# Optimization experiments

Hardware: AMD Instinct MI355X
Metric: run time of the kernel (lower is better)

The kernel has to match this reference:

```python
import jax, jax.numpy as jnp
import numpy as np

N_NODES = 100000   # number of graph nodes
N_EDGES = 1600000  # adjacency nnz (avg degree 16)
FEAT_NNZ = 1600000 # sparse feature nnz (~16 per node)
F_IN = 512
F_OUT = 128


def setup_inputs() -> dict:
    key = jax.random.key(0)
    k1, k2, k3, k4, k5, k6 = jax.random.split(key, 6)
    adj_indices = jax.random.randint(k1, (2, N_EDGES), 0, N_NODES, dtype=jnp.int64 if jax.config.jax_enable_x64 else jnp.int32)
    adj_values = jax.random.uniform(k2, (N_EDGES,), dtype=jnp.float32)
    feat_rows = jax.random.randint(k3, (FEAT_NNZ,), 0, N_NODES)
    feat_cols = jax.random.randint(k4, (FEAT_NNZ,), 0, F_IN)
    feat_values = jax.random.uniform(k5, (FEAT_NNZ,), dtype=jnp.float32)
    # xavier_uniform init of the dense weight, as in the torch module
    bound = float(np.sqrt(6.0 / (F_IN + F_OUT)))
    weight = jax.random.uniform(k6, (F_IN, F_OUT), dtype=jnp.float32, minval=-bound, maxval=bound)
    return {
        "adj_indices": adj_indices,
        "adj_values": adj_values,
        "feat_rows": feat_rows,
        "feat_cols": feat_cols,
        "feat_values": feat_values,
        "weight": weight,
        "num_nodes": N_NODES,
    }


def _spmm(rows, cols, vals, num_rows, dense):
    """COO sparse [num_rows, ?] @ dense [?, K] -> [num_rows, K]."""
    msgs = vals[:, None] * dense[cols]          # [nnz, K] gather + scale
    return jax.ops.segment_sum(msgs, rows, num_segments=num_rows)


def reference(adj_indices, adj_values, feat_rows, feat_cols, feat_values, weight, num_nodes):
    # spmm(features, W): sparse [N, F_in] @ [F_in, F_out]
    base_features = _spmm(feat_rows, feat_cols, feat_values, num_nodes, weight)
    # spmm(A_hat, base): sparse [N, N] @ [N, F_out]  -- neighbor aggregation
    out = _spmm(adj_indices[0], adj_indices[1], adj_values, num_nodes, base_features)
    return out
```

## Files before the change

kernel.cpp:

```cpp
#include <hip/hip_runtime.h>
#include <stdint.h>

#define N_NODES 100000
#define F_IN    512
#define F_OUT   128
#define BROWS   128
#define NBKT    ((N_NODES + BROWS - 1) / BROWS)
#define CAP     2560
#define EPB     4096
#define BR2     64
#define SCAP    1536

typedef unsigned short     u16;
typedef unsigned int       u32;
typedef unsigned long long u64;
typedef long long          i64;

__device__ __forceinline__ float b2f(u16 u) {
    union { u32 i; float f; } x; x.i = ((u32)u) << 16; return x.f;
}
__device__ __forceinline__ u16 f2b(float f) {
    u32 i = __float_as_uint(f);
    return (u16)((i + 0x7fffu + ((i >> 16) & 1u)) >> 16);
}
__device__ __forceinline__ float blo(u32 u) { return __uint_as_float(u << 16); }
__device__ __forceinline__ float bhi(u32 u) { return __uint_as_float(u & 0xFFFF0000u); }
__device__ __forceinline__ int ld_idx(const void* p, int i, int w64) {
    return w64 ? (int)((const i64*)p)[i] : ((const int*)p)[i];
}
__device__ __forceinline__ u16 ld_val_bf(const void* p, int i, int f32) {
    return f32 ? f2b(((const float*)p)[i]) : ((const u16*)p)[i];
}

__global__ void sniff_k(const u16* __restrict__ w, const u32* __restrict__ adj,
                        const u32* __restrict__ frows, int* __restrict__ flags,
                        int* __restrict__ gcurF, int* __restrict__ gcurA) {
    int t = threadIdx.x;
    if (t < 64) {
        int lane = t;
        u32 e0 = (w[lane]      >> 7) & 0xFF;
        u32 e1 = (w[64 + lane] >> 7) & 0xFF;
        u64 bad = __ballot((e0 > 0x7B) || (e1 > 0x7B));
        u64 za = __ballot(adj[2 * lane + 1] == 0u);
        u64 zf = __ballot(frows[2 * lane + 1] == 0u);
        if (lane == 0) {
            flags[0] = (bad != 0);
            flags[1] = (__popcll(za) >= 32);
            flags[2] = (__popcll(zf) >= 32);
        }
    }
    for (int i = t; i < NBKT; i += 256) { gcurF[i] = 0; gcurA[i] = 0; }
}

__global__ __launch_bounds__(256) void binFA_k(
        const void* __restrict__ frows, const void* __restrict__ fcols,
        const void* __restrict__ fvals, int M, int nFb,
        const void* __restrict__ adjbase, const void* __restrict__ avals, int E,
        const int* __restrict__ flags,
        int* __restrict__ gcurF, int* __restrict__ gcurA,
        u32* __restrict__ fbkt, u64* __restrict__ abkt) {
    __shared__ int hist[NBKT];
    __shared__ int hbase[NBKT];
    int t = threadIdx.x;
    for (int i = t; i < NBKT; i += 256) hist[i] = 0;
    __syncthreads();
    int f32 = flags[0];
    if ((int)blockIdx.x < nFb) {
        int f64 = flags[2];
        int start = blockIdx.x * EPB;
        int end = min(start + EPB, M);
        for (int i = start + t; i < end; i += 256)
            atomicAdd(&hist[ld_idx(frows, i, f64) >> 7], 1);
        __syncthreads();
        for (int i = t; i < NBKT; i += 256) {
            int h = hist[i];
            hbase[i] = h ? atomicAdd(&gcurF[i], h) : 0;
            hist[i] = 0;
        }
        __syncthreads();
        for (int i = start + t; i < end; i += 256) {
            int r = ld_idx(frows, i, f64);
            int c = ld_idx(fcols, i, f64);
            u32 v = ld_val_bf(fvals, i, f32);
            int b = r >> 7;
            int pos = hbase[b] + atomicAdd(&hist[b], 1);
            if (pos < CAP)
                fbkt[(size_t)b * CAP + pos] = (v << 16) | ((u32)(r & 127) << 9) | (u32)c;
        }
    } else {
        int a64 = flags[1];
        const void* acols = a64 ? (const void*)((const i64*)adjbase + E)
                                : (const void*)((const int*)adjbase + E);
        int start = ((int)blockIdx.x - nFb) * EPB;
        int end = min(start + EPB, E);
        for (int i = start + t; i < end; i += 256)
            atomicAdd(&hist[ld_idx(adjbase, i, a64) >> 7], 1);
        __syncthreads();
        for (int i = t; i < NBKT; i += 256) {
            int h = hist[i];
            hbase[i] = h ? atomicAdd(&gcurA[i], h) : 0;
            hist[i] = 0;
        }
        __syncthreads();
        for (int i = start + t; i < end; i += 256) {
            int r = ld_idx(adjbase, i, a64);
            int c = ld_idx(acols, i, a64);
            u64 v = ld_val_bf(avals, i, f32);
            int b = r >> 7;
            int pos = hbase[b] + atomicAdd(&hist[b], 1);
            if (pos < CAP)
                abkt[(size_t)b * CAP + pos] = (v << 24) | ((u64)(r & 127) << 17) | (u64)(u32)c;
        }
    }
}

__global__ __launch_bounds__(256, 8) void stage1_k(const int* __restrict__ cnt,
        const u32* __restrict__ bkts, const void* __restrict__ W,
        const int* __restrict__ flags, u16* __restrict__ base) {
    __shared__ u32 csr[SCAP];
    __shared__ int hcnt[BR2];
    __shared__ int roff[BR2 + 1];
    __shared__ int cur[BR2];
    int t = threadIdx.x;
    int b = blockIdx.x >> 1;
    int half = blockIdx.x & 1;
    int n = cnt[b]; if (n > CAP) n = CAP;
    const u32* ed = bkts + (size_t)b * CAP;
    if (t < BR2) hcnt[t] = 0;
    __syncthreads();
    for (int i = t; i < n; i += 256) {
        int rl = (ed[i] >> 9) & 0x7F;
        if ((rl >> 6) == half) atomicAdd(&hcnt[rl & 63], 1);
    }
    __syncthreads();
    if (t < 64) {
        int h = hcnt[t];
        int v = h;
        #pragma unroll
        for (int off = 1; off < 64; off <<= 1) {
            int u = __shfl_up(v, off);
            if (t >= off) v += u;
        }
        roff[t + 1] = v;
        cur[t] = v - h;
        if (t == 0) roff[0] = 0;
    }
    __syncthreads();
    for (int i = t; i < n; i += 256) {
        u32 p = ed[i];
        int rl = (p >> 9) & 0x7F;
        if ((rl >> 6) == half) {
            int pos = atomicAdd(&cur[rl & 63], 1);
            if (pos < SCAP) csr[pos] = p;
        }
    }
    __syncthreads();
    int wave = t >> 6, lane = t & 63, g = lane >> 4, l16 = lane & 15;
    int f32 = flags[0];
    #pragma unroll
    for (int set = 0; set < 4; ++set) {
        int row = set * 16 + wave * 4 + g;
        int s = roff[row], e = roff[row + 1];
        if (s > SCAP) s = SCAP;
        if (e > SCAP) e = SCAP;
        float a[8] = {0.f, 0.f, 0.f, 0.f, 0.f, 0.f, 0.f, 0.f};
        if (f32) {
            const float* Wf = (const float*)W;
            for (int j0 = s; j0 < e; j0 += 4) {
                u32 p[4]; float4 qa[4], qb[4];
                #pragma unroll
                for (int k = 0; k < 4; ++k) { int jk = j0 + k; p[k] = csr[jk < e ? jk : e - 1]; }
                #pragma unroll
                for (int k = 0; k < 4; ++k) {
                    const float* wp = Wf + (size_t)(p[k] & 0x1FF) * F_OUT + l16 * 8;
                    qa[k] = *(const float4*)wp;
                    qb[k] = *(const float4*)(wp + 4);
                }
                #pragma unroll
                for (int k = 0; k < 4; ++k) {
                    float v = (j0 + k < e) ? b2f((u16)(p[k] >> 16)) : 0.f;
                    a[0] += v * qa[k].x; a[1] += v * qa[k].y;
                    a[2] += v * qa[k].z; a[3] += v * qa[k].w;
                    a[4] += v * qb[k].x; a[5] += v * qb[k].y;
                    a[6] += v * qb[k].z; a[7] += v * qb[k].w;
                }
            }
        } else {
            const u16* Wb = (const u16*)W;
            for (int j0 = s; j0 < e; j0 += 4) {
                u32 p[4]; uint4 q[4];
                #pragma unroll
                for (int k = 0; k < 4; ++k) { int jk = j0 + k; p[k] = csr[jk < e ? jk : e - 1]; }
                #pragma unroll
                for (int k = 0; k < 4; ++k)
                    q[k] = *(const uint4*)(Wb + (size_t)(p[k] & 0x1FF) * F_OUT + l16 * 8);
                #pragma unroll
                for (int k = 0; k < 4; ++k) {
                    float v = (j0 + k < e) ? b2f((u16)(p[k] >> 16)) : 0.f;
                    a[0] += v * blo(q[k].x); a[1] += v * bhi(q[k].x);
                    a[2] += v * blo(q[k].y); a[3] += v * bhi(q[k].y);
                    a[4] += v * blo(q[k].z); a[5] += v * bhi(q[k].z);
                    a[6] += v * blo(q[k].w); a[7] += v * bhi(q[k].w);
                }
            }
        }
        int gr = b * BROWS + half * BR2 + row;
        if (gr < N_NODES) {
            uint4 o;
            o.x = (u32)f2b(a[0]) | ((u32)f2b(a[1]) << 16);
            o.y = (u32)f2b(a[2]) | ((u32)f2b(a[3]) << 16);
            o.z = (u32)f2b(a[4]) | ((u32)f2b(a[5]) << 16);
            o.w = (u32)f2b(a[6]) | ((u32)f2b(a[7]) << 16);
            *(uint4*)(base + (size_t)gr * F_OUT + l16 * 8) = o;
        }
    }
}

__global__ __launch_bounds__(256, 8) void stage2_k(const int* __restrict__ cnt,
        const u64* __restrict__ bkts, const u16* __restrict__ base,
        const int* __restrict__ flags, void* __restrict__ out) {
    __shared__ u64 csr[SCAP];
    __shared__ int hcnt[BR2];
    __shared__ int roff[BR2 + 1];
    __shared__ int cur[BR2];
    int t = threadIdx.x;
    int b = blockIdx.x >> 1;
    int half = blockIdx.x & 1;
    int n = cnt[b]; if (n > CAP) n = CAP;
    const u64* ed = bkts + (size_t)b * CAP;
    if (t < BR2) hcnt[t] = 0;
    __syncthreads();
    for (int i = t; i < n; i += 256) {
        int rl = (int)((ed[i] >> 17) & 0x7F);
        if ((rl >> 6) == half) atomicAdd(&hcnt[rl & 63], 1);
    }
    __syncthreads();
    if (t < 64) {
        int h = hcnt[t];
        int v = h;
        #pragma unroll
        for (int off = 1; off < 64; off <<= 1) {
            int u = __shfl_up(v, off);
            if (t >= off) v += u;
        }
        roff[t + 1] = v;
        cur[t] = v - h;
        if (t == 0) roff[0] = 0;
    }
    __syncthreads();
    for (int i = t; i < n; i += 256) {
        u64 p = ed[i];
        int rl = (int)((p >> 17) & 0x7F);
        if ((rl >> 6) == half) {
            int pos = atomicAdd(&cur[rl & 63], 1);
            if (pos < SCAP) csr[pos] = p;
        }
    }
    __syncthreads();
    int wave = t >> 6, lane = t & 63, g = lane >> 4, l16 = lane & 15;
    int f32o = flags[0];
    #pragma unroll
    for (int set = 0; set < 4; ++set) {
        int row = set * 16 + wave * 4 + g;
        int s = roff[row], e = roff[row + 1];
        if (s > SCAP) s = SCAP;
        if (e > SCAP) e = SCAP;
        float a[8] = {0.f, 0.f, 0.f, 0.f, 0.f, 0.f, 0.f, 0.f};
        for (int j0 = s; j0 < e; j0 += 4) {
            u64 p[4]; uint4 q[4];
            #pragma unroll
            for (int k = 0; k < 4; ++k) { int jk = j0 + k; p[k] = csr[jk < e ? jk : e - 1]; }
            #pragma unroll
            for (int k = 0; k < 4; ++k)
                q[k] = *(const uint4*)(base + (size_t)(u32)(p[k] & 0x1FFFF) * F_OUT + l16 * 8);
            #pragma unroll
            for (int k = 0; k < 4; ++k) {
                float v = (j0 + k < e) ? b2f((u16)(p[k] >> 24)) : 0.f;
                a[0] += v * blo(q[k].x); a[1] += v * bhi(q[k].x);
                a[2] += v * blo(q[k].y); a[3] += v * bhi(q[k].y);
                a[4] += v * blo(q[k].z); a[5] += v * bhi(q[k].z);
                a[6] += v * blo(q[k].w); a[7] += v * bhi(q[k].w);
            }
        }
        int gr = b * BROWS + half * BR2 + row;
        if (gr < N_NODES) {
            if (f32o) {
                float* op = (float*)out + (size_t)gr * F_OUT + l16 * 8;
                float4 o0, o1;
                o0.x = a[0]; o0.y = a[1]; o0.z = a[2]; o0.w = a[3];
                o1.x = a[4]; o1.y = a[5]; o1.z = a[6]; o1.w = a[7];
                *(float4*)op = o0;
                *(float4*)(op + 4) = o1;
            } else {
                uint4 o;
                o.x = (u32)f2b(a[0]) | ((u32)f2b(a[1]) << 16);
                o.y = (u32)f2b(a[2]) | ((u32)f2b(a[3]) << 16);
                o.z = (u32)f2b(a[4]) | ((u32)f2b(a[5]) << 16);
                o.w = (u32)f2b(a[6]) | ((u32)f2b(a[7]) << 16);
                *(uint4*)((u16*)out + (size_t)gr * F_OUT + l16 * 8) = o;
            }
        }
    }
}

extern "C" void kernel_launch(void* const* d_in, const int* in_sizes, int n_in,
                              void* d_out, int out_size, void* d_ws, size_t ws_size,
                              hipStream_t stream) {
    const void* adj_idx   = d_in[0];
    const void* adj_vals  = d_in[1];
    const void* feat_rows = d_in[2];
    const void* feat_cols = d_in[3];
    const void* feat_vals = d_in[4];
    const void* weight    = d_in[5];

    const int E = in_sizes[0] / 2;
    const int M = in_sizes[2];

    char* ws = (char*)d_ws;
    size_t o = 0;
    auto alloc = [&](size_t b) { size_t r = o; o += (b + 255) & ~(size_t)255; return r; };
    int* gcurF = (int*)(ws + alloc((size_t)NBKT * 4));
    int* gcurA = (int*)(ws + alloc((size_t)NBKT * 4));
    int* flags = (int*)(ws + alloc(4 * 4));
    u32* fbkt  = (u32*)(ws + alloc((size_t)NBKT * CAP * 4));
    u64* abkt  = (u64*)(ws + alloc((size_t)NBKT * CAP * 8));
    u16* base  = (u16*)(ws + alloc((size_t)N_NODES * F_OUT * 2));
    (void)ws_size;

    const int nFb = (M + EPB - 1) / EPB;
    const int nAb = (E + EPB - 1) / EPB;

    sniff_k<<<1, 256, 0, stream>>>((const u16*)weight, (const u32*)adj_idx,
                                   (const u32*)feat_rows, flags, gcurF, gcurA);
    binFA_k<<<nFb + nAb, 256, 0, stream>>>(feat_rows, feat_cols, feat_vals, M, nFb,
                                           adj_idx, adj_vals, E,
                                           flags, gcurF, gcurA, fbkt, abkt);
    stage1_k<<<2 * NBKT, 256, 0, stream>>>(gcurF, fbkt, weight, flags, base);
    stage2_k<<<2 * NBKT, 256, 0, stream>>>(gcurA, abkt, base, flags, d_out);
}
```

Measured before the change: 280.2 us.

## Stage binned entries in shared memory sorted by bucket before global scatter

The binning kernel now computes a block-local exclusive scan of the bucket histogram. It scatters each packed entry into a shared-memory buffer sorted by bucket, then writes to the global bucket arrays in sorted order, so consecutive threads mostly hit consecutive addresses. This replaces fully random global scatter writes with mostly coalesced ones. In exchange it uses about 40KB of extra LDS per block (u64 sort buffer plus u16 bucket tags), which lowers occupancy, and adds a scan plus another barrier pass.

```diff
diff --git a/kernel.cpp b/kernel.cpp
--- a/kernel.cpp
+++ b/kernel.cpp
@@ -59,12 +59,18 @@
         const int* __restrict__ flags,
         int* __restrict__ gcurF, int* __restrict__ gcurA,
         u32* __restrict__ fbkt, u64* __restrict__ abkt) {
+    __shared__ u64 sortA[EPB];
+    __shared__ u16 sbkt[EPB];
     __shared__ int hist[NBKT];
+    __shared__ int lbase[NBKT];
     __shared__ int hbase[NBKT];
+    __shared__ int wtot[4];
     int t = threadIdx.x;
+    int lane = t & 63, wv = t >> 6;
     for (int i = t; i < NBKT; i += 256) hist[i] = 0;
     __syncthreads();
     int f32 = flags[0];
+
     if ((int)blockIdx.x < nFb) {
         int f64 = flags[2];
         int start = blockIdx.x * EPB;
@@ -72,20 +78,55 @@
         for (int i = start + t; i < end; i += 256)
             atomicAdd(&hist[ld_idx(frows, i, f64) >> 7], 1);
         __syncthreads();
-        for (int i = t; i < NBKT; i += 256) {
-            int h = hist[i];
-            hbase[i] = h ? atomicAdd(&gcurF[i], h) : 0;
-            hist[i] = 0;
-        }
-        __syncthreads();
+        {
+            int b0 = t * 4;
+            int c0 = (b0 + 0 < NBKT) ? hist[b0 + 0] : 0;
+            int c1 = (b0 + 1 < NBKT) ? hist[b0 + 1] : 0;
+            int c2 = (b0 + 2 < NBKT) ? hist[b0 + 2] : 0;
+            int c3 = (b0 + 3 < NBKT) ? hist[b0 + 3] : 0;
+            int s = c0 + c1 + c2 + c3;
+            int v = s;
+            #pragma unroll
+            for (int off = 1; off < 64; off <<= 1) {
+                int u = __shfl_up(v, off);
+                if (lane >= off) v += u;
+            }
+            if (lane == 63) wtot[wv] = v;
+            __syncthreads();
+            int woff = 0;
+            #pragma unroll
+            for (int w = 0; w < 4; ++w) if (w < wv) woff += wtot[w];
+            int run = woff + v - s;
+            int cc[4] = {c0, c1, c2, c3};
+            #pragma unroll
+            for (int k = 0; k < 4; ++k) {
+                int bb = b0 + k;
+                if (bb < NBKT) {
+                    lbase[bb] = run;
+                    hist[bb] = run;
+                    hbase[bb] = cc[k] ? atomicAdd(&gcurF[bb], cc[k]) : 0;
+                    run += cc[k];
+                }
+            }
+        }
+        __syncthreads();
+        u32* sortF = (u32*)sortA;
         for (int i = start + t; i < end; i += 256) {
             int r = ld_idx(frows, i, f64);
             int c = ld_idx(fcols, i, f64);
             u32 v = ld_val_bf(fvals, i, f32);
             int b = r >> 7;
-            int pos = hbase[b] + atomicAdd(&hist[b], 1);
+            int pos = atomicAdd(&hist[b], 1);
+            sortF[pos] = (v << 16) | ((u32)(r & 127) << 9) | (u32)c;
+            sbkt[pos] = (u16)b;
+        }
+        __syncthreads();
+        int n = end - start;
+        for (int i = t; i < n; i += 256) {
+            int b = sbkt[i];
+            int pos = hbase[b] + (i - lbase[b]);
             if (pos < CAP)
-                fbkt[(size_t)b * CAP + pos] = (v << 16) | ((u32)(r & 127) << 9) | (u32)c;
+                fbkt[(size_t)b * CAP + pos] = sortF[i];
         }
     } else {
         int a64 = flags[1];
@@ -96,10 +137,36 @@
         for (int i = start + t; i < end; i += 256)
             atomicAdd(&hist[ld_idx(adjbase, i, a64) >> 7], 1);
         __syncthreads();
-        for (int i = t; i < NBKT; i += 256) {
-            int h = hist[i];
-            hbase[i] = h ? atomicAdd(&gcurA[i], h) : 0;
-            hist[i] = 0;
+        {
+            int b0 = t * 4;
+            int c0 = (b0 + 0 < NBKT) ? hist[b0 + 0] : 0;
+            int c1 = (b0 + 1 < NBKT) ? hist[b0 + 1] : 0;
+            int c2 = (b0 + 2 < NBKT) ? hist[b0 + 2] : 0;
+            int c3 = (b0 + 3 < NBKT) ? hist[b0 + 3] : 0;
+            int s = c0 + c1 + c2 + c3;
+            int v = s;
+            #pragma unroll
+            for (int off = 1; off < 64; off <<= 1) {
+                int u = __shfl_up(v, off);
+                if (lane >= off) v += u;
+            }
+            if (lane == 63) wtot[wv] = v;
+            __syncthreads();
+            int woff = 0;
+            #pragma unroll
+            for (int w = 0; w < 4; ++w) if (w < wv) woff += wtot[w];
+            int run = woff + v - s;
+            int cc[4] = {c0, c1, c2, c3};
+            #pragma unroll
+            for (int k = 0; k < 4; ++k) {
+                int bb = b0 + k;
+                if (bb < NBKT) {
+                    lbase[bb] = run;
+                    hist[bb] = run;
+                    hbase[bb] = cc[k] ? atomicAdd(&gcurA[bb], cc[k]) : 0;
+                    run += cc[k];
+                }
+            }
         }
         __syncthreads();
         for (int i = start + t; i < end; i += 256) {
@@ -107,9 +174,17 @@
             int c = ld_idx(acols, i, a64);
             u64 v = ld_val_bf(avals, i, f32);
             int b = r >> 7;
-            int pos = hbase[b] + atomicAdd(&hist[b], 1);
+            int pos = atomicAdd(&hist[b], 1);
+            sortA[pos] = (v << 24) | ((u64)(r & 127) << 17) | (u64)(u32)c;
+            sbkt[pos] = (u16)b;
+        }
+        __syncthreads();
+        int n = end - start;
+        for (int i = t; i < n; i += 256) {
+            int b = sbkt[i];
+            int pos = hbase[b] + (i - lbase[b]);
             if (pos < CAP)
-                abkt[(size_t)b * CAP + pos] = (v << 24) | ((u64)(r & 127) << 17) | (u64)(u32)c;
+                abkt[(size_t)b * CAP + pos] = sortA[i];
         }
     }
 }
```

Measured after the change: 280.7 us. No clear change (+0.2%).

## Split feature binning, fuse adjacency binning with stage1, use full-bucket 512-thread blocks

Applied to the files above, without the earlier changes.

Feature binning now runs in its own kernel, and adjacency binning is merged with the stage-1 feature SpMM in one launch whose blocks share memory through a union, so the two independent phases can overlap. The binning kernels load four edges per thread with vectorized loads, using 2048-edge blocks of 512 threads. Stage 1 and stage 2 now process a whole 128-row bucket per 512-thread block rather than splitting it in halves, which drops the duplicated bucket scans, and the gather loops are unrolled by 8. The cost is larger shared memory per block, lower occupancy limits, and more registers from the wider unroll. The SCAP clamp on csr writes is removed, so csr now relies on n being clamped to CAP.

```diff
diff --git a/kernel.cpp b/kernel.cpp
--- a/kernel.cpp
+++ b/kernel.cpp
@@ -7,9 +7,7 @@
 #define BROWS   128
 #define NBKT    ((N_NODES + BROWS - 1) / BROWS)
 #define CAP     2560
-#define EPB     4096
-#define BR2     64
-#define SCAP    1536
+#define EPB     2048
 
 typedef unsigned short     u16;
 typedef unsigned int       u32;
@@ -30,6 +28,26 @@
 }
 __device__ __forceinline__ u16 ld_val_bf(const void* p, int i, int f32) {
     return f32 ? f2b(((const float*)p)[i]) : ((const u16*)p)[i];
+}
+__device__ __forceinline__ void ld_idx4(int* r, const void* p, int g, int w64) {
+    if (w64) {
+        const i64* q = (const i64*)p + 4 * (size_t)g;
+        longlong2 a = *(const longlong2*)q;
+        longlong2 b = *(const longlong2*)(q + 2);
+        r[0] = (int)a.x; r[1] = (int)a.y; r[2] = (int)b.x; r[3] = (int)b.y;
+    } else {
+        int4 a = *(const int4*)((const int*)p + 4 * (size_t)g);
+        r[0] = a.x; r[1] = a.y; r[2] = a.z; r[3] = a.w;
+    }
+}
+__device__ __forceinline__ void ld_val4(u32* v, const void* p, int g, int f32) {
+    if (f32) {
+        float4 a = *(const float4*)((const float*)p + 4 * (size_t)g);
+        v[0] = f2b(a.x); v[1] = f2b(a.y); v[2] = f2b(a.z); v[3] = f2b(a.w);
+    } else {
+        ushort4 a = *(const ushort4*)((const u16*)p + 4 * (size_t)g);
+        v[0] = a.x; v[1] = a.y; v[2] = a.z; v[3] = a.w;
+    }
 }
 
 __global__ void sniff_k(const u16* __restrict__ w, const u32* __restrict__ adj,
@@ -37,13 +55,12 @@
                         int* __restrict__ gcurF, int* __restrict__ gcurA) {
     int t = threadIdx.x;
     if (t < 64) {
-        int lane = t;
-        u32 e0 = (w[lane]      >> 7) & 0xFF;
-        u32 e1 = (w[64 + lane] >> 7) & 0xFF;
+        u32 e0 = (w[t]      >> 7) & 0xFF;
+        u32 e1 = (w[64 + t] >> 7) & 0xFF;
         u64 bad = __ballot((e0 > 0x7B) || (e1 > 0x7B));
-        u64 za = __ballot(adj[2 * lane + 1] == 0u);
-        u64 zf = __ballot(frows[2 * lane + 1] == 0u);
-        if (lane == 0) {
+        u64 za = __ballot(adj[2 * t + 1] == 0u);
+        u64 zf = __ballot(frows[2 * t + 1] == 0u);
+        if (t == 0) {
             flags[0] = (bad != 0);
             flags[1] = (__popcll(za) >= 32);
             flags[2] = (__popcll(zf) >= 32);
@@ -52,124 +69,154 @@
     for (int i = t; i < NBKT; i += 256) { gcurF[i] = 0; gcurA[i] = 0; }
 }
 
-__global__ __launch_bounds__(256) void binFA_k(
-        const void* __restrict__ frows, const void* __restrict__ fcols,
-        const void* __restrict__ fvals, int M, int nFb,
-        const void* __restrict__ adjbase, const void* __restrict__ avals, int E,
-        const int* __restrict__ flags,
-        int* __restrict__ gcurF, int* __restrict__ gcurA,
-        u32* __restrict__ fbkt, u64* __restrict__ abkt) {
+__global__ __launch_bounds__(512, 6) void binF_k(const void* __restrict__ frows,
+        const void* __restrict__ fcols, const void* __restrict__ fvals, int M,
+        const int* __restrict__ flags, int* __restrict__ gcurF, u32* __restrict__ fbkt) {
     __shared__ int hist[NBKT];
     __shared__ int hbase[NBKT];
     int t = threadIdx.x;
-    for (int i = t; i < NBKT; i += 256) hist[i] = 0;
-    __syncthreads();
+    for (int i = t; i < NBKT; i += 512) hist[i] = 0;
+    __syncthreads();
+    int f64 = flags[2], f32 = flags[0];
+    int start = blockIdx.x * EPB;
+    int end = min(start + EPB, M);
+    int g = (start >> 2) + t;
+    int e0 = 4 * g;
+    int r[4] = {-1, -1, -1, -1};
+    int c[4]; u32 v[4];
+    if (e0 + 3 < end) {
+        ld_idx4(r, frows, g, f64);
+        ld_idx4(c, fcols, g, f64);
+        ld_val4(v, fvals, g, f32);
+    } else {
+        #pragma unroll
+        for (int j = 0; j < 4; ++j) if (e0 + j < end) {
+            r[j] = ld_idx(frows, e0 + j, f64);
+            c[j] = ld_idx(fcols, e0 + j, f64);
+            v[j] = ld_val_bf(fvals, e0 + j, f32);
+        }
+    }
+    #pragma unroll
+    for (int j = 0; j < 4; ++j) if (r[j] >= 0) atomicAdd(&hist[r[j] >> 7], 1);
+    __syncthreads();
+    for (int i = t; i < NBKT; i += 512) {
+        int h = hist[i];
+        hbase[i] = h ? atomicAdd(&gcurF[i], h) : 0;
+        hist[i] = 0;
+    }
+    __syncthreads();
+    #pragma unroll
+    for (int j = 0; j < 4; ++j) if (r[j] >= 0) {
+        int b = r[j] >> 7;
+        int pos = hbase[b] + atomicAdd(&hist[b], 1);
+        if (pos < CAP)
+            fbkt[(size_t)b * CAP + pos] = (v[j] << 16) | ((u32)(r[j] & 127) << 9) | (u32)c[j];
+    }
+}
+
+union S1Mem {
+    struct { int hist[NBKT]; int hbase[NBKT]; } bin;
+    struct { u32 csr[CAP]; int hcnt[BROWS]; int roff[BROWS + 1]; int cur[BROWS]; } s1;
+};
+
+__global__ __launch_bounds__(512, 4) void binA_s1_k(
+        const void* __restrict__ adjbase, const void* __restrict__ avals, int E, int nAb,
+        const int* __restrict__ flags, int* __restrict__ gcurA, u64* __restrict__ abkt,
+        const int* __restrict__ cntF, const u32* __restrict__ fbkt,
+        const void* __restrict__ W, u16* __restrict__ base) {
+    __shared__ S1Mem sm;
+    int t = threadIdx.x;
     int f32 = flags[0];
-    if ((int)blockIdx.x < nFb) {
-        int f64 = flags[2];
-        int start = blockIdx.x * EPB;
-        int end = min(start + EPB, M);
-        for (int i = start + t; i < end; i += 256)
-            atomicAdd(&hist[ld_idx(frows, i, f64) >> 7], 1);
+    if ((int)blockIdx.x < nAb) {
+        for (int i = t; i < NBKT; i += 512) sm.bin.hist[i] = 0;
         __syncthreads();
-        for (int i = t; i < NBKT; i += 256) {
-            int h = hist[i];
-            hbase[i] = h ? atomicAdd(&gcurF[i], h) : 0;
-            hist[i] = 0;
-        }
-        __syncthreads();
-        for (int i = start + t; i < end; i += 256) {
-            int r = ld_idx(frows, i, f64);
-            int c = ld_idx(fcols, i, f64);
-            u32 v = ld_val_bf(fvals, i, f32);
-            int b = r >> 7;
-            int pos = hbase[b] + atomicAdd(&hist[b], 1);
-            if (pos < CAP)
-                fbkt[(size_t)b * CAP + pos] = (v << 16) | ((u32)(r & 127) << 9) | (u32)c;
-        }
-    } else {
         int a64 = flags[1];
         const void* acols = a64 ? (const void*)((const i64*)adjbase + E)
                                 : (const void*)((const int*)adjbase + E);
-        int start = ((int)blockIdx.x - nFb) * EPB;
+        int start = blockIdx.x * EPB;
         int end = min(start + EPB, E);
-        for (int i = start + t; i < end; i += 256)
-            atomicAdd(&hist[ld_idx(adjbase, i, a64) >> 7], 1);
+        int g = (start >> 2) + t;
+        int e0 = 4 * g;
+        int r[4] = {-1, -1, -1, -1};
+        int c[4]; u32 v[4];
+        if (e0 + 3 < end) {
+            ld_idx4(r, adjbase, g, a64);
+            ld_idx4(c, acols, g, a64);
+            ld_val4(v, avals, g, f32);
+        } else {
+            #pragma unroll
+            for (int j = 0; j < 4; ++j) if (e0 + j < end) {
+                r[j] = ld_idx(adjbase, e0 + j, a64);
+                c[j] = ld_idx(acols, e0 + j, a64);
+                v[j] = ld_val_bf(avals, e0 + j, f32);
+            }
+        }
+        #pragma unroll
+        for (int j = 0; j < 4; ++j) if (r[j] >= 0) atomicAdd(&sm.bin.hist[r[j] >> 7], 1);
         __syncthreads();
-        for (int i = t; i < NBKT; i += 256) {
-            int h = hist[i];
-            hbase[i] = h ? atomicAdd(&gcurA[i], h) : 0;
-            hist[i] = 0;
+        for (int i = t; i < NBKT; i += 512) {
+            int h = sm.bin.hist[i];
+            sm.bin.hbase[i] = h ? atomicAdd(&gcurA[i], h) : 0;
+            sm.bin.hist[i] = 0;
         }
         __syncthreads();
-        for (int i = start + t; i < end; i += 256) {
-            int r = ld_idx(adjbase, i, a64);
-            int c = ld_idx(acols, i, a64);
-            u64 v = ld_val_bf(avals, i, f32);
-            int b = r >> 7;
-            int pos = hbase[b] + atomicAdd(&hist[b], 1);
+        #pragma unroll
+        for (int j = 0; j < 4; ++j) if (r[j] >= 0) {
+            int b = r[j] >> 7;
+            int pos = sm.bin.hbase[b] + atomicAdd(&sm.bin.hist[b], 1);
             if (pos < CAP)
-                abkt[(size_t)b * CAP + pos] = (v << 24) | ((u64)(r & 127) << 17) | (u64)(u32)c;
-        }
-    }
-}
-
-__global__ __launch_bounds__(256, 8) void stage1_k(const int* __restrict__ cnt,
-        const u32* __restrict__ bkts, const void* __restrict__ W,
-        const int* __restrict__ flags, u16* __restrict__ base) {
-    __shared__ u32 csr[SCAP];
-    __shared__ int hcnt[BR2];
-    __shared__ int roff[BR2 + 1];
-    __shared__ int cur[BR2];
-    int t = threadIdx.x;
-    int b = blockIdx.x >> 1;
-    int half = blockIdx.x & 1;
-    int n = cnt[b]; if (n > CAP) n = CAP;
-    const u32* ed = bkts + (size_t)b * CAP;
-    if (t < BR2) hcnt[t] = 0;
-    __syncthreads();
-    for (int i = t; i < n; i += 256) {
-        int rl = (ed[i] >> 9) & 0x7F;
-        if ((rl >> 6) == half) atomicAdd(&hcnt[rl & 63], 1);
-    }
+                abkt[(size_t)b * CAP + pos] =
+                    ((u64)v[j] << 24) | ((u64)(r[j] & 127) << 17) | (u64)(u32)c[j];
+        }
+        return;
+    }
+    int b = blockIdx.x - nAb;
+    int n = cntF[b]; if (n > CAP) n = CAP;
+    const u32* ed = fbkt + (size_t)b * CAP;
+    if (t < BROWS) sm.s1.hcnt[t] = 0;
+    __syncthreads();
+    u32 pb[5];
+    #pragma unroll
+    for (int k = 0; k < 5; ++k) { int i = t + k * 512; pb[k] = (i < n) ? ed[i] : 0u; }
+    #pragma unroll
+    for (int k = 0; k < 5; ++k) { int i = t + k * 512; if (i < n) atomicAdd(&sm.s1.hcnt[(pb[k] >> 9) & 127], 1); }
     __syncthreads();
     if (t < 64) {
-        int h = hcnt[t];
-        int v = h;
+        int h0 = sm.s1.hcnt[2 * t], h1 = sm.s1.hcnt[2 * t + 1];
+        int s = h0 + h1, v2 = s;
         #pragma unroll
         for (int off = 1; off < 64; off <<= 1) {
-            int u = __shfl_up(v, off);
-            if (t >= off) v += u;
-        }
-        roff[t + 1] = v;
-        cur[t] = v - h;
-        if (t == 0) roff[0] = 0;
-    }
-    __syncthreads();
-    for (int i = t; i < n; i += 256) {
-        u32 p = ed[i];
-        int rl = (p >> 9) & 0x7F;
-        if ((rl >> 6) == half) {
-            int pos = atomicAdd(&cur[rl & 63], 1);
-            if (pos < SCAP) csr[pos] = p;
-        }
-    }
-    __syncthreads();
-    int wave = t >> 6, lane = t & 63, g = lane >> 4, l16 = lane & 15;
-    int f32 = flags[0];
+            int u = __shfl_up(v2, off);
+            if (t >= off) v2 += u;
+        }
+        int excl = v2 - s;
+        sm.s1.roff[2 * t] = excl;     sm.s1.roff[2 * t + 1] = excl + h0;
+        sm.s1.cur[2 * t]  = excl;     sm.s1.cur[2 * t + 1]  = excl + h0;
+        if (t == 63) sm.s1.roff[128] = v2;
+    }
+    __syncthreads();
+    #pragma unroll
+    for (int k = 0; k < 5; ++k) {
+        int i = t + k * 512;
+        if (i < n) {
+            u32 p = pb[k];
+            int pos = atomicAdd(&sm.s1.cur[(p >> 9) & 127], 1);
+            sm.s1.csr[pos] = p;
+        }
+    }
+    __syncthreads();
+    int wave = t >> 6, lane = t & 63, g16 = lane >> 4, l16 = lane & 15;
     #pragma unroll
     for (int set = 0; set < 4; ++set) {
-        int row = set * 16 + wave * 4 + g;
-        int s = roff[row], e = roff[row + 1];
-        if (s > SCAP) s = SCAP;
-        if (e > SCAP) e = SCAP;
+        int row = set * 32 + wave * 4 + g16;
+        int s = sm.s1.roff[row], e = sm.s1.roff[row + 1];
         float a[8] = {0.f, 0.f, 0.f, 0.f, 0.f, 0.f, 0.f, 0.f};
         if (f32) {
             const float* Wf = (const float*)W;
             for (int j0 = s; j0 < e; j0 += 4) {
                 u32 p[4]; float4 qa[4], qb[4];
                 #pragma unroll
-                for (int k = 0; k < 4; ++k) { int jk = j0 + k; p[k] = csr[jk < e ? jk : e - 1]; }
+                for (int k = 0; k < 4; ++k) { int jk = j0 + k; p[k] = sm.s1.csr[jk < e ? jk : e - 1]; }
                 #pragma unroll
                 for (int k = 0; k < 4; ++k) {
                     const float* wp = Wf + (size_t)(p[k] & 0x1FF) * F_OUT + l16 * 8;
@@ -187,15 +234,15 @@
             }
         } else {
             const u16* Wb = (const u16*)W;
-            for (int j0 = s; j0 < e; j0 += 4) {
-                u32 p[4]; uint4 q[4];
-                #pragma unroll
-                for (int k = 0; k < 4; ++k) { int jk = j0 + k; p[k] = csr[jk < e ? jk : e - 1]; }
-                #pragma unroll
-                for (int k = 0; k < 4; ++k)
+            for (int j0 = s; j0 < e; j0 += 8) {
+                u32 p[8]; uint4 q[8];
+                #pragma unroll
+                for (int k = 0; k < 8; ++k) { int jk = j0 + k; p[k] = sm.s1.csr[jk < e ? jk : e - 1]; }
+                #pragma unroll
+                for (int k = 0; k < 8; ++k)
                     q[k] = *(const uint4*)(Wb + (size_t)(p[k] & 0x1FF) * F_OUT + l16 * 8);
                 #pragma unroll
-                for (int k = 0; k < 4; ++k) {
+                for (int k = 0; k < 8; ++k) {
                     float v = (j0 + k < e) ? b2f((u16)(p[k] >> 16)) : 0.f;
                     a[0] += v * blo(q[k].x); a[1] += v * bhi(q[k].x);
                     a[2] += v * blo(q[k].y); a[3] += v * bhi(q[k].y);
@@ -204,7 +251,7 @@
                 }
             }
         }
-        int gr = b * BROWS + half * BR2 + row;
+        int gr = b * BROWS + row;
         if (gr < N_NODES) {
             uint4 o;
             o.x = (u32)f2b(a[0]) | ((u32)f2b(a[1]) << 16);
@@ -216,65 +263,65 @@
     }
 }
 
-__global__ __launch_bounds__(256, 8) void stage2_k(const int* __restrict__ cnt,
+__global__ __launch_bounds__(512, 4) void stage2_k(const int* __restrict__ cnt,
         const u64* __restrict__ bkts, const u16* __restrict__ base,
         const int* __restrict__ flags, void* __restrict__ out) {
-    __shared__ u64 csr[SCAP];
-    __shared__ int hcnt[BR2];
-    __shared__ int roff[BR2 + 1];
-    __shared__ int cur[BR2];
+    __shared__ u64 csr[CAP];
+    __shared__ int hcnt[BROWS];
+    __shared__ int roff[BROWS + 1];
+    __shared__ int cur[BROWS];
     int t = threadIdx.x;
-    int b = blockIdx.x >> 1;
-    int half = blockIdx.x & 1;
+    int b = blockIdx.x;
     int n = cnt[b]; if (n > CAP) n = CAP;
     const u64* ed = bkts + (size_t)b * CAP;
-    if (t < BR2) hcnt[t] = 0;
-    __syncthreads();
-    for (int i = t; i < n; i += 256) {
-        int rl = (int)((ed[i] >> 17) & 0x7F);
-        if ((rl >> 6) == half) atomicAdd(&hcnt[rl & 63], 1);
-    }
+    if (t < BROWS) hcnt[t] = 0;
+    __syncthreads();
+    u64 pb[5];
+    #pragma unroll
+    for (int k = 0; k < 5; ++k) { int i = t + k * 512; pb[k] = (i < n) ? ed[i] : 0ull; }
+    #pragma unroll
+    for (int k = 0; k < 5; ++k) { int i = t + k * 512; if (i < n) atomicAdd(&hcnt[(int)((pb[k] >> 17) & 127)], 1); }
     __syncthreads();
     if (t < 64) {
-        int h = hcnt[t];
-        int v = h;
+        int h0 = hcnt[2 * t], h1 = hcnt[2 * t + 1];
+        int s = h0 + h1, v2 = s;
         #pragma unroll
         for (int off = 1; off < 64; off <<= 1) {
-            int u = __shfl_up(v, off);
-            if (t >= off) v += u;
-        }
-        roff[t + 1] = v;
-        cur[t] = v - h;
-        if (t == 0) roff[0] = 0;
-    }
-    __syncthreads();
-    for (int i = t; i < n; i += 256) {
-        u64 p = ed[i];
-        int rl = (int)((p >> 17) & 0x7F);
-        if ((rl >> 6) == half) {
-            int pos = atomicAdd(&cur[rl & 63], 1);
-            if (pos < SCAP) csr[pos] = p;
-        }
-    }
-    __syncthreads();
-    int wave = t >> 6, lane = t & 63, g = lane >> 4, l16 = lane & 15;
+            int u = __shfl_up(v2, off);
+            if (t >= off) v2 += u;
+        }
+        int excl = v2 - s;
+        roff[2 * t] = excl;     roff[2 * t + 1] = excl + h0;
+        cur[2 * t]  = excl;     cur[2 * t + 1]  = excl + h0;
+        if (t == 63) roff[128] = v2;
+    }
+    __syncthreads();
+    #pragma unroll
+    for (int k = 0; k < 5; ++k) {
+        int i = t + k * 512;
+        if (i < n) {
+            u64 p = pb[k];
+            int pos = atomicAdd(&cur[(int)((p >> 17) & 127)], 1);
+            csr[pos] = p;
+        }
+    }
+    __syncthreads();
+    int wave = t >> 6, lane = t & 63, g16 = lane >> 4, l16 = lane & 15;
     int f32o = flags[0];
     #pragma unroll
     for (int set = 0; set < 4; ++set) {
-        int row = set * 16 + wave * 4 + g;
+        int row = set * 32 + wave * 4 + g16;
         int s = roff[row], e = roff[row + 1];
-        if (s > SCAP) s = SCAP;
-        if (e > SCAP) e = SCAP;
         float a[8] = {0.f, 0.f, 0.f, 0.f, 0.f, 0.f, 0.f, 0.f};
-        for (int j0 = s; j0 < e; j0 += 4) {
-            u64 p[4]; uint4 q[4];
+        for (int j0 = s; j0 < e; j0 += 8) {
+            u64 p[8]; uint4 q[8];
             #pragma unroll
-            for (int k = 0; k < 4; ++k) { int jk = j0 + k; p[k] = csr[jk < e ? jk : e - 1]; }
+            for (int k = 0; k < 8; ++k) { int jk = j0 + k; p[k] = csr[jk < e ? jk : e - 1]; }
             #pragma unroll
-            for (int k = 0; k < 4; ++k)
+            for (int k = 0; k < 8; ++k)
                 q[k] = *(const uint4*)(base + (size_t)(u32)(p[k] & 0x1FFFF) * F_OUT + l16 * 8);
             #pragma unroll
-            for (int k = 0; k < 4; ++k) {
+            for (int k = 0; k < 8; ++k) {
                 float v = (j0 + k < e) ? b2f((u16)(p[k] >> 24)) : 0.f;
                 a[0] += v * blo(q[k].x); a[1] += v * bhi(q[k].x);
                 a[2] += v * blo(q[k].y); a[3] += v * bhi(q[k].y);
@@ -282,7 +329,7 @@
                 a[6] += v * blo(q[k].w); a[7] += v * bhi(q[k].w);
             }
         }
-        int gr = b * BROWS + half * BR2 + row;
+        int gr = b * BROWS + row;
         if (gr < N_NODES) {
             if (f32o) {
                 float* op = (float*)out + (size_t)gr * F_OUT + l16 * 8;
@@ -332,9 +379,10 @@
 
     sniff_k<<<1, 256, 0, stream>>>((const u16*)weight, (const u32*)adj_idx,
                                    (const u32*)feat_rows, flags, gcurF, gcurA);
-    binFA_k<<<nFb + nAb, 256, 0, stream>>>(feat_rows, feat_cols, feat_vals, M, nFb,
-                                           adj_idx, adj_vals, E,
-                                           flags, gcurF, gcurA, fbkt, abkt);
-    stage1_k<<<2 * NBKT, 256, 0, stream>>>(gcurF, fbkt, weight, flags, base);
-    stage2_k<<<2 * NBKT, 256, 0, stream>>>(gcurA, abkt, base, flags, d_out);
-}
+    binF_k<<<nFb, 512, 0, stream>>>(feat_rows, feat_cols, feat_vals, M,
+                                    flags, gcurF, fbkt);
+    binA_s1_k<<<nAb + NBKT, 512, 0, stream>>>(adj_idx, adj_vals, E, nAb,
+                                              flags, gcurA, abkt,
+                                              gcurF, fbkt, weight, base);
+    stage2_k<<<NBKT, 512, 0, stream>>>(gcurA, abkt, base, flags, d_out);
+}
```

Measured after the change: 262.8 us. -6.2%, faster.
